# Optimization experiments

Measured on AMD Instinct MI355X. Metric: run time of the kernel, lower is better.

Reference implementation:

```python
import jax, jax.numpy as jnp
import numpy as np

N, K, R = 32768, 4096, 256

def setup_inputs() -> dict:
    key = jax.random.key(0)
    k1, k2, k3 = jax.random.split(key, 3)
    H = jax.random.normal(k1, (N, R), dtype=jnp.float32)
    L = jax.random.normal(k2, (K, R), dtype=jnp.float32)
    W_I = jax.random.normal(k3, (R, R), dtype=jnp.float32)
    return {"H": H, "L": L, "W_I": W_I}

def reference(H, L, W_I):
    # Q = W_I @ L^T : (r, k)
    Q = jnp.einsum('rs,ks->rk', W_I, L)
    # M_I = H @ Q : (n, k)
    M_I = jnp.einsum('nr,rk->nk', H, Q)
    A_I = jax.nn.softmax(M_I, axis=1)
    # C_I = A_I @ L : (n, r)
    C_I = jnp.einsum('nk,kr->nr', A_I, L)
    return (C_I, A_I)
```

## Files before the change

kernel.cpp:

```cpp
#include <hip/hip_runtime.h>
#include <hip/hip_bf16.h>
#include <math.h>
#include <stdint.h>

constexpr int N_ROWS = 32768;
constexpr int K_DIM  = 4096;
constexpr int R_DIM  = 256;
constexpr int KP     = 3 * R_DIM;
constexpr int KB     = K_DIM / 128;

typedef __bf16 bf16x8 __attribute__((ext_vector_type(8)));
typedef float  f32x4  __attribute__((ext_vector_type(4)));
typedef unsigned short u16x8 __attribute__((ext_vector_type(8)));
typedef unsigned short u16x4 __attribute__((ext_vector_type(4)));

__device__ __forceinline__ unsigned short f2bf(float x) {
    unsigned u = __float_as_uint(x);
    u += 0x7fffu + ((u >> 16) & 1u);
    return (unsigned short)(u >> 16);
}
__device__ __forceinline__ float bf2f(unsigned short h) {
    return __uint_as_float((unsigned)h << 16);
}

__device__ __forceinline__ void gl2lds16(const void* gptr, void* lptr) {
    __builtin_amdgcn_global_load_lds(
        (const __attribute__((address_space(1))) unsigned int*)gptr,
        (__attribute__((address_space(3))) unsigned int*)lptr,
        16, 0, 0);
}

__global__ __launch_bounds__(256)
void gemm_mfma_nt(const unsigned short* __restrict__ A,
                  const unsigned short* __restrict__ B,
                  float* __restrict__ C,
                  float* __restrict__ Pm, float* __restrict__ Ps,
                  int M, int N, int Kc)
{
    __shared__ __align__(16) unsigned short As[128 * 32];
    __shared__ __align__(16) unsigned short Bs[128 * 32];
    __shared__ float pm_s[128][2], ps_s[128][2];

    const int tid  = threadIdx.x;
    const int wave = tid >> 6, lane = tid & 63;
    const int wm = wave >> 1, wn = wave & 1;
    const long m0 = (long)blockIdx.x * 128;
    const long n0 = (long)blockIdx.y * 128;

    f32x4 acc[4][4] = {};

    const int srow  = lane >> 2;
    const int skoff = (lane & 3) * 8;
    const int c0 = wave, c1 = wave + 4;
    const int kq = (lane >> 4) * 8;
    const int mr = lane & 15;

    for (int k0 = 0; k0 < Kc; k0 += 32) {
        gl2lds16(A + (m0 + c0 * 16 + srow) * (long)Kc + k0 + skoff, &As[c0 * 512]);
        gl2lds16(A + (m0 + c1 * 16 + srow) * (long)Kc + k0 + skoff, &As[c1 * 512]);
        gl2lds16(B + (n0 + c0 * 16 + srow) * (long)Kc + k0 + skoff, &Bs[c0 * 512]);
        gl2lds16(B + (n0 + c1 * 16 + srow) * (long)Kc + k0 + skoff, &Bs[c1 * 512]);
        __syncthreads();

        bf16x8 af[4], bfr[4];
#pragma unroll
        for (int t = 0; t < 4; ++t) {
            af[t]  = *(const bf16x8*)&As[(wm * 64 + t * 16 + mr) * 32 + kq];
            bfr[t] = *(const bf16x8*)&Bs[(wn * 64 + t * 16 + mr) * 32 + kq];
        }
#pragma unroll
        for (int i = 0; i < 4; ++i)
#pragma unroll
            for (int j = 0; j < 4; ++j)
                acc[i][j] = __builtin_amdgcn_mfma_f32_16x16x32_bf16(
                    af[i], bfr[j], acc[i][j], 0, 0, 0);
        __syncthreads();
    }

    const int col = lane & 15, rquad = (lane >> 4) * 4;
#pragma unroll
    for (int i = 0; i < 4; ++i) {
        const long mrow = m0 + wm * 64 + i * 16 + rquad;
#pragma unroll
        for (int j = 0; j < 4; ++j) {
            float* p = C + mrow * (long)N + n0 + wn * 64 + j * 16 + col;
#pragma unroll
            for (int r = 0; r < 4; ++r) p[(long)r * N] = acc[i][j][r];
        }
    }

#pragma unroll
    for (int i = 0; i < 4; ++i) {
#pragma unroll
        for (int r = 0; r < 4; ++r) {
            float mx = fmaxf(fmaxf(acc[i][0][r], acc[i][1][r]),
                             fmaxf(acc[i][2][r], acc[i][3][r]));
#pragma unroll
            for (int off = 1; off < 16; off <<= 1)
                mx = fmaxf(mx, __shfl_xor(mx, off));
            float sm = 0.f;
#pragma unroll
            for (int j = 0; j < 4; ++j) sm += __expf(acc[i][j][r] - mx);
#pragma unroll
            for (int off = 1; off < 16; off <<= 1)
                sm += __shfl_xor(sm, off);
            if (mr == 0) {
                const int rw = wm * 64 + i * 16 + rquad + r;
                pm_s[rw][wn] = mx;
                ps_s[rw][wn] = sm;
            }
        }
    }
    __syncthreads();
    if (tid < 128) {
        const float ma = pm_s[tid][0], mb = pm_s[tid][1];
        const float mx = fmaxf(ma, mb);
        const float s  = ps_s[tid][0] * __expf(ma - mx) +
                         ps_s[tid][1] * __expf(mb - mx);
        Pm[(m0 + tid) * KB + blockIdx.y] = mx;
        Ps[(m0 + tid) * KB + blockIdx.y] = s;
    }
}

__global__ __launch_bounds__(256)
void finalize_ms(const float* __restrict__ Pm, const float* __restrict__ Ps,
                 float* __restrict__ SMm, float* __restrict__ SMi)
{
    const long row = (long)blockIdx.x * 256 + threadIdx.x;
    const float4* pm = (const float4*)(Pm + row * KB);
    const float4* ps = (const float4*)(Ps + row * KB);
    float4 v[8];
    float mx = -3.4e38f;
#pragma unroll
    for (int q = 0; q < 8; ++q) {
        v[q] = pm[q];
        mx = fmaxf(mx, fmaxf(fmaxf(v[q].x, v[q].y), fmaxf(v[q].z, v[q].w)));
    }
    float s = 0.f;
#pragma unroll
    for (int q = 0; q < 8; ++q) {
        float4 w = ps[q];
        s += w.x * __expf(v[q].x - mx) + w.y * __expf(v[q].y - mx) +
             w.z * __expf(v[q].z - mx) + w.w * __expf(v[q].w - mx);
    }
    SMm[row] = mx;
    SMi[row] = 1.f / s;
}

__global__ __launch_bounds__(256)
void softmax_av_sp(float* __restrict__ Mio,
                   const unsigned short* __restrict__ LT,
                   const float* __restrict__ SMm, const float* __restrict__ SMi,
                   float* __restrict__ C)
{
    __shared__ __align__(16) unsigned short Bs[2][R_DIM * 32];
    __shared__ __align__(16) unsigned short As[2][32 * 32];
    __shared__ float sm_m[32], sm_inv[32];

    const int tid  = threadIdx.x;
    const int wave = tid >> 6, lane = tid & 63;
    const long m0 = (long)blockIdx.x * 32;

    if (tid < 32) { sm_m[tid] = SMm[m0 + tid]; sm_inv[tid] = SMi[m0 + tid]; }
    __syncthreads();

    const int mr   = lane & 15;
    const int kq16 = (lane >> 4) * 16;
    const int arow = tid >> 3;
    const int acol = (tid & 7) * 4;
    const int abyte = (arow * 64 + (tid & 7) * 8) ^ ((arow & 3) << 4);
    const float myM = sm_m[arow], myI = sm_inv[arow];
    float* const arp = Mio + (m0 + arow) * (long)K_DIM + acol;

    f32x4 acc[2][4] = {};

    auto stage_B = [&](int buf, int kk0) {
#pragma unroll
        for (int w = 0; w < 4; ++w) {
            const int rloc = wave * 64 + w * 16 + (lane >> 2);
            const int sb   = ((lane & 3) * 16) ^ ((rloc & 3) << 4);
            gl2lds16((const char*)LT + (long)rloc * (K_DIM * 2) + (long)kk0 * 2 + sb,
                     &Bs[buf][(wave * 64 + w * 16) * 32]);
        }
    };
    auto emit_A = [&](int buf, int kk0, float4 v) {
        const float e0 = __expf(v.x - myM), e1 = __expf(v.y - myM);
        const float e2 = __expf(v.z - myM), e3 = __expf(v.w - myM);
        *(float4*)(arp + kk0) = make_float4(e0 * myI, e1 * myI, e2 * myI, e3 * myI);
        u16x4 u;
        u[0] = f2bf(e0); u[1] = f2bf(e1); u[2] = f2bf(e2); u[3] = f2bf(e3);
        *(u16x4*)((char*)As[buf] + abyte) = u;
    };

    stage_B(0, 0);
    emit_A(0, 0, *(const float4*)(arp + 0));
    __syncthreads();

    int cur = 0;
    for (int t = 0; t < K_DIM / 32; ++t) {
        const int nxt = cur ^ 1;
        float4 vn;
        const bool has_next = (t < K_DIM / 32 - 1);
        if (has_next) {
            stage_B(nxt, (t + 1) * 32);
            vn = *(const float4*)(arp + (t + 1) * 32);
        }

        bf16x8 af[2], bfr[4];
#pragma unroll
        for (int q = 0; q < 2; ++q) {
            const int ar = q * 16 + mr;
            af[q] = *(const bf16x8*)((const char*)As[cur] +
                    ((ar * 64 + kq16) ^ ((ar & 3) << 4)));
        }
#pragma unroll
        for (int q = 0; q < 4; ++q) {
            const int br = wave * 64 + q * 16 + mr;
            bfr[q] = *(const bf16x8*)((const char*)Bs[cur] +
                     ((br * 64 + kq16) ^ ((br & 3) << 4)));
        }
#pragma unroll
        for (int i = 0; i < 2; ++i)
#pragma unroll
            for (int j = 0; j < 4; ++j)
                acc[i][j] = __builtin_amdgcn_mfma_f32_16x16x32_bf16(
                    af[i], bfr[j], acc[i][j], 0, 0, 0);

        if (has_next) emit_A(nxt, (t + 1) * 32, vn);
        __syncthreads();
        cur = nxt;
    }

    const int col = lane & 15, rquad = (lane >> 4) * 4;
#pragma unroll
    for (int i = 0; i < 2; ++i) {
        const int lrow0 = i * 16 + rquad;
#pragma unroll
        for (int j = 0; j < 4; ++j) {
            float* p = C + (m0 + lrow0) * (long)R_DIM + wave * 64 + j * 16 + col;
#pragma unroll
            for (int r = 0; r < 4; ++r)
                p[(long)r * R_DIM] = acc[i][j][r] * sm_inv[lrow0 + r];
        }
    }
}

__global__ __launch_bounds__(256)
void prep_B(const float* __restrict__ L, unsigned short* __restrict__ Bp)
{
    const long i = (long)blockIdx.x * 256 + threadIdx.x;
    const long k = i >> 8; const int r = (int)(i & 255);
    const float x = L[i];
    const unsigned short hi = f2bf(x);
    const unsigned short lo = f2bf(x - bf2f(hi));
    unsigned short* row = Bp + k * KP;
    row[r] = hi; row[R_DIM + r] = lo; row[2 * R_DIM + r] = hi;
}

__global__ __launch_bounds__(256)
void prep_LT(const float* __restrict__ L, unsigned short* __restrict__ LT)
{
    const long i = (long)blockIdx.x * 256 + threadIdx.x;
    const long r = i >> 12; const long k = i & 4095;
    LT[r * K_DIM + k] = f2bf(L[k * R_DIM + r]);
}

template<bool BT>
__global__ __launch_bounds__(256)
void gemm128(const float* __restrict__ A, const float* __restrict__ B,
             float* __restrict__ C, int M, int N, int Kc)
{
    __shared__ __align__(16) float Asl[16][132];
    __shared__ __align__(16) float Bsl[16][132];

    const int tid = threadIdx.x;
    const int tx = tid & 15, ty = tid >> 4;
    const long m0 = (long)blockIdx.x * 128;
    const long n0 = (long)blockIdx.y * 128;

    float acc[8][8];
#pragma unroll
    for (int i = 0; i < 8; ++i)
#pragma unroll
        for (int j = 0; j < 8; ++j) acc[i][j] = 0.f;

    for (int k0 = 0; k0 < Kc; k0 += 16) {
#pragma unroll
        for (int q = 0; q < 2; ++q) {
            int fi = tid + 256 * q, row = fi >> 2, col = (fi & 3) * 4;
            float4 v = *(const float4*)(A + (m0 + row) * (long)Kc + k0 + col);
            Asl[col + 0][row] = v.x; Asl[col + 1][row] = v.y;
            Asl[col + 2][row] = v.z; Asl[col + 3][row] = v.w;
        }
        if (BT) {
#pragma unroll
            for (int q = 0; q < 2; ++q) {
                int fi = tid + 256 * q, row = fi >> 2, col = (fi & 3) * 4;
                float4 v = *(const float4*)(B + (n0 + row) * (long)Kc + k0 + col);
                Bsl[col + 0][row] = v.x; Bsl[col + 1][row] = v.y;
                Bsl[col + 2][row] = v.z; Bsl[col + 3][row] = v.w;
            }
        } else {
#pragma unroll
            for (int q = 0; q < 2; ++q) {
                int fi = tid + 256 * q, row = fi >> 5, col = (fi & 31) * 4;
                float4 v = *(const float4*)(B + (k0 + row) * (long)N + n0 + col);
                *(float4*)&Bsl[row][col] = v;
            }
        }
        __syncthreads();
#pragma unroll
        for (int kk = 0; kk < 16; ++kk) {
            float a[8], b[8];
            *(float4*)&a[0] = *(const float4*)&Asl[kk][ty * 8];
            *(float4*)&a[4] = *(const float4*)&Asl[kk][ty * 8 + 4];
            *(float4*)&b[0] = *(const float4*)&Bsl[kk][tx * 8];
            *(float4*)&b[4] = *(const float4*)&Bsl[kk][tx * 8 + 4];
#pragma unroll
            for (int i = 0; i < 8; ++i)
#pragma unroll
                for (int j = 0; j < 8; ++j)
                    acc[i][j] = fmaf(a[i], b[j], acc[i][j]);
        }
        __syncthreads();
    }
#pragma unroll
    for (int i = 0; i < 8; ++i) {
        float* p = C + (m0 + ty * 8 + i) * (long)N + n0 + tx * 8;
        *(float4*)p       = make_float4(acc[i][0], acc[i][1], acc[i][2], acc[i][3]);
        *(float4*)(p + 4) = make_float4(acc[i][4], acc[i][5], acc[i][6], acc[i][7]);
    }
}

__global__ __launch_bounds__(256)
void gemm128_hl(const float* __restrict__ A, const float* __restrict__ B,
                unsigned short* __restrict__ Ap, int M, int N, int Kc)
{
    __shared__ __align__(16) float Asl[16][132];
    __shared__ __align__(16) float Bsl[16][132];

    const int tid = threadIdx.x;
    const int tx = tid & 15, ty = tid >> 4;
    const long m0 = (long)blockIdx.x * 128;
    const long n0 = (long)blockIdx.y * 128;

    float acc[8][8];
#pragma unroll
    for (int i = 0; i < 8; ++i)
#pragma unroll
        for (int j = 0; j < 8; ++j) acc[i][j] = 0.f;

    for (int k0 = 0; k0 < Kc; k0 += 16) {
#pragma unroll
        for (int q = 0; q < 2; ++q) {
            int fi = tid + 256 * q, row = fi >> 2, col = (fi & 3) * 4;
            float4 v = *(const float4*)(A + (m0 + row) * (long)Kc + k0 + col);
            Asl[col + 0][row] = v.x; Asl[col + 1][row] = v.y;
            Asl[col + 2][row] = v.z; Asl[col + 3][row] = v.w;
        }
#pragma unroll
        for (int q = 0; q < 2; ++q) {
            int fi = tid + 256 * q, row = fi >> 5, col = (fi & 31) * 4;
            float4 v = *(const float4*)(B + (k0 + row) * (long)N + n0 + col);
            *(float4*)&Bsl[row][col] = v;
        }
        __syncthreads();
#pragma unroll
        for (int kk = 0; kk < 16; ++kk) {
            float a[8], b[8];
            *(float4*)&a[0] = *(const float4*)&Asl[kk][ty * 8];
            *(float4*)&a[4] = *(const float4*)&Asl[kk][ty * 8 + 4];
            *(float4*)&b[0] = *(const float4*)&Bsl[kk][tx * 8];
            *(float4*)&b[4] = *(const float4*)&Bsl[kk][tx * 8 + 4];
#pragma unroll
            for (int i = 0; i < 8; ++i)
#pragma unroll
                for (int j = 0; j < 8; ++j)
                    acc[i][j] = fmaf(a[i], b[j], acc[i][j]);
        }
        __syncthreads();
    }
#pragma unroll
    for (int i = 0; i < 8; ++i) {
        const long row = m0 + ty * 8 + i;
        const int  cb  = (int)n0 + tx * 8;
        u16x8 vh, vl;
#pragma unroll
        for (int j = 0; j < 8; ++j) {
            const float x = acc[i][j];
            const unsigned short hi = f2bf(x);
            vh[j] = hi;
            vl[j] = f2bf(x - bf2f(hi));
        }
        unsigned short* rp = Ap + row * KP;
        *(u16x8*)(rp + cb)             = vh;
        *(u16x8*)(rp + R_DIM + cb)     = vh;
        *(u16x8*)(rp + 2 * R_DIM + cb) = vl;
    }
}

__global__ __launch_bounds__(256)
void softmax_rows(float* __restrict__ Mio)
{
    const long n  = blockIdx.x;
    float* row    = Mio + n * (long)K_DIM;
    const int tid = threadIdx.x;

    float4 v[4];
    float lmax = -3.4e38f;
#pragma unroll
    for (int q = 0; q < 4; ++q) {
        v[q] = ((const float4*)row)[tid + 256 * q];
        lmax = fmaxf(lmax, fmaxf(fmaxf(v[q].x, v[q].y), fmaxf(v[q].z, v[q].w)));
    }
    __shared__ float redmax[4], redsum[4];
#pragma unroll
    for (int off = 32; off > 0; off >>= 1)
        lmax = fmaxf(lmax, __shfl_xor(lmax, off));
    if ((tid & 63) == 0) redmax[tid >> 6] = lmax;
    __syncthreads();
    const float gmax = fmaxf(fmaxf(redmax[0], redmax[1]), fmaxf(redmax[2], redmax[3]));

    float lsum = 0.f;
#pragma unroll
    for (int q = 0; q < 4; ++q) {
        v[q].x = __expf(v[q].x - gmax); v[q].y = __expf(v[q].y - gmax);
        v[q].z = __expf(v[q].z - gmax); v[q].w = __expf(v[q].w - gmax);
        lsum += v[q].x + v[q].y + v[q].z + v[q].w;
    }
#pragma unroll
    for (int off = 32; off > 0; off >>= 1)
        lsum += __shfl_xor(lsum, off);
    if ((tid & 63) == 0) redsum[tid >> 6] = lsum;
    __syncthreads();
    const float inv = 1.f / (redsum[0] + redsum[1] + redsum[2] + redsum[3]);
#pragma unroll
    for (int q = 0; q < 4; ++q) {
        v[q].x *= inv; v[q].y *= inv; v[q].z *= inv; v[q].w *= inv;
        ((float4*)row)[tid + 256 * q] = v[q];
    }
}

extern "C" void kernel_launch(void* const* d_in, const int* in_sizes, int n_in,
                              void* d_out, int out_size, void* d_ws, size_t ws_size,
                              hipStream_t stream)
{
    const float* H  = (const float*)d_in[0];
    const float* L  = (const float*)d_in[1];
    const float* Wi = (const float*)d_in[2];

    float* Cout = (float*)d_out;
    float* Aout = (float*)d_out + (size_t)N_ROWS * R_DIM;

    const size_t szAp = (size_t)N_ROWS * KP * 2;
    const size_t szBp = (size_t)K_DIM * KP * 2;
    const size_t szLT = (size_t)R_DIM * K_DIM * 2;
    const size_t szPm = (size_t)N_ROWS * KB * 4;
    const size_t szPs = (size_t)N_ROWS * KB * 4;
    const size_t szSM = (size_t)N_ROWS * 4;

    if (ws_size >= szAp + szBp + szLT + szPm + szPs + 2 * szSM) {
        char* w = (char*)d_ws;
        unsigned short* Ap = (unsigned short*)w;                 w += szAp;
        unsigned short* Bp = (unsigned short*)w;                 w += szBp;
        unsigned short* LT = (unsigned short*)w;                 w += szLT;
        float* Pm  = (float*)w;                                  w += szPm;
        float* Ps  = (float*)w;                                  w += szPs;
        float* SMm = (float*)w;                                  w += szSM;
        float* SMi = (float*)w;

        gemm128_hl<<<dim3(N_ROWS / 128, R_DIM / 128), 256, 0, stream>>>(
            H, Wi, Ap, N_ROWS, R_DIM, R_DIM);
        prep_B<<<dim3((K_DIM * R_DIM) / 256), 256, 0, stream>>>(L, Bp);
        prep_LT<<<dim3((R_DIM * K_DIM) / 256), 256, 0, stream>>>(L, LT);
        gemm_mfma_nt<<<dim3(N_ROWS / 128, K_DIM / 128), 256, 0, stream>>>(
            Ap, Bp, Aout, Pm, Ps, N_ROWS, K_DIM, KP);
        finalize_ms<<<dim3(N_ROWS / 256), 256, 0, stream>>>(Pm, Ps, SMm, SMi);
        softmax_av_sp<<<dim3(N_ROWS / 32), 256, 0, stream>>>(
            Aout, LT, SMm, SMi, Cout);
    } else {
        gemm128<false><<<dim3(N_ROWS / 128, R_DIM / 128), 256, 0, stream>>>(
            H, Wi, Cout, N_ROWS, R_DIM, R_DIM);
        gemm128<true><<<dim3(N_ROWS / 128, K_DIM / 128), 256, 0, stream>>>(
            Cout, L, Aout, N_ROWS, K_DIM, R_DIM);
        softmax_rows<<<dim3(N_ROWS), 256, 0, stream>>>(Aout);
        gemm128<false><<<dim3(N_ROWS / 128, R_DIM / 128), 256, 0, stream>>>(
            Aout, L, Cout, N_ROWS, R_DIM, K_DIM);
    }
}
```

Measured before the change: 1.359 ms.

## Load B operands directly from global memory and widen softmax-AV tiles

The first GEMM no longer stages the small B matrix in LDS. Each wave loads its B fragments straight from global memory, which relies on L2 reuse, and the grid is swapped so blocks sharing an A row-tile run together. The softmax-AV kernel moves to 512 threads covering 64 rows and 64-wide K steps. It also drops the LDS staging of L^T in favour of direct global loads, cutting LDS traffic and barriers per step. The risk is uncoalesced, latency-exposed global loads for B in place of the shared-memory reuse.

```diff
diff --git a/kernel.cpp b/kernel.cpp
--- a/kernel.cpp
+++ b/kernel.cpp
@@ -38,14 +38,13 @@
                   int M, int N, int Kc)
 {
     __shared__ __align__(16) unsigned short As[128 * 32];
-    __shared__ __align__(16) unsigned short Bs[128 * 32];
     __shared__ float pm_s[128][2], ps_s[128][2];
 
     const int tid  = threadIdx.x;
     const int wave = tid >> 6, lane = tid & 63;
     const int wm = wave >> 1, wn = wave & 1;
-    const long m0 = (long)blockIdx.x * 128;
-    const long n0 = (long)blockIdx.y * 128;
+    const long m0 = (long)blockIdx.y * 128;
+    const long n0 = (long)blockIdx.x * 128;
 
     f32x4 acc[4][4] = {};
 
@@ -55,19 +54,23 @@
     const int kq = (lane >> 4) * 8;
     const int mr = lane & 15;
 
+    const unsigned short* const Bbase = B + n0 * (long)Kc + kq;
+
     for (int k0 = 0; k0 < Kc; k0 += 32) {
         gl2lds16(A + (m0 + c0 * 16 + srow) * (long)Kc + k0 + skoff, &As[c0 * 512]);
         gl2lds16(A + (m0 + c1 * 16 + srow) * (long)Kc + k0 + skoff, &As[c1 * 512]);
-        gl2lds16(B + (n0 + c0 * 16 + srow) * (long)Kc + k0 + skoff, &Bs[c0 * 512]);
-        gl2lds16(B + (n0 + c1 * 16 + srow) * (long)Kc + k0 + skoff, &Bs[c1 * 512]);
-        __syncthreads();
-
-        bf16x8 af[4], bfr[4];
-#pragma unroll
-        for (int t = 0; t < 4; ++t) {
-            af[t]  = *(const bf16x8*)&As[(wm * 64 + t * 16 + mr) * 32 + kq];
-            bfr[t] = *(const bf16x8*)&Bs[(wn * 64 + t * 16 + mr) * 32 + kq];
-        }
+
+        bf16x8 bfr[4];
+#pragma unroll
+        for (int t = 0; t < 4; ++t)
+            bfr[t] = *(const bf16x8*)(Bbase + (wn * 64 + t * 16 + mr) * (long)Kc + k0);
+
+        __syncthreads();
+
+        bf16x8 af[4];
+#pragma unroll
+        for (int t = 0; t < 4; ++t)
+            af[t] = *(const bf16x8*)&As[(wm * 64 + t * 16 + mr) * 32 + kq];
 #pragma unroll
         for (int i = 0; i < 4; ++i)
 #pragma unroll
@@ -117,8 +120,8 @@
         const float mx = fmaxf(ma, mb);
         const float s  = ps_s[tid][0] * __expf(ma - mx) +
                          ps_s[tid][1] * __expf(mb - mx);
-        Pm[(m0 + tid) * KB + blockIdx.y] = mx;
-        Ps[(m0 + tid) * KB + blockIdx.y] = s;
+        Pm[(m0 + tid) * KB + blockIdx.x] = mx;
+        Ps[(m0 + tid) * KB + blockIdx.x] = s;
     }
 }
 
@@ -147,86 +150,88 @@
     SMi[row] = 1.f / s;
 }
 
-__global__ __launch_bounds__(256)
-void softmax_av_sp(float* __restrict__ Mio,
-                   const unsigned short* __restrict__ LT,
-                   const float* __restrict__ SMm, const float* __restrict__ SMi,
-                   float* __restrict__ C)
-{
-    __shared__ __align__(16) unsigned short Bs[2][R_DIM * 32];
-    __shared__ __align__(16) unsigned short As[2][32 * 32];
-    __shared__ float sm_m[32], sm_inv[32];
+__global__ __launch_bounds__(512)
+void softmax_av2(float* __restrict__ Mio,
+                 const unsigned short* __restrict__ LT,
+                 const float* __restrict__ SMm, const float* __restrict__ SMi,
+                 float* __restrict__ C)
+{
+    __shared__ __align__(16) unsigned short As[2][64 * 64];
+    __shared__ float sm_m[64], sm_inv[64];
 
     const int tid  = threadIdx.x;
     const int wave = tid >> 6, lane = tid & 63;
-    const long m0 = (long)blockIdx.x * 32;
-
-    if (tid < 32) { sm_m[tid] = SMm[m0 + tid]; sm_inv[tid] = SMi[m0 + tid]; }
+    const long m0 = (long)blockIdx.x * 64;
+
+    if (tid < 64) { sm_m[tid] = SMm[m0 + tid]; sm_inv[tid] = SMi[m0 + tid]; }
     __syncthreads();
 
-    const int mr   = lane & 15;
+    const int wm = wave >> 2, wn = wave & 3;
+    const int mr = lane & 15;
+    const int kq   = (lane >> 4) * 8;
     const int kq16 = (lane >> 4) * 16;
-    const int arow = tid >> 3;
-    const int acol = (tid & 7) * 4;
-    const int abyte = (arow * 64 + (tid & 7) * 8) ^ ((arow & 3) << 4);
+
+    const int arow  = tid >> 3;
+    const int abyte = (arow * 128 + (tid & 7) * 16) ^ ((arow & 7) << 4);
     const float myM = sm_m[arow], myI = sm_inv[arow];
-    float* const arp = Mio + (m0 + arow) * (long)K_DIM + acol;
+    float* const arp = Mio + (m0 + arow) * (long)K_DIM + (tid & 7) * 8;
+
+    const unsigned short* const Lbase = LT + (wn * 64) * (long)K_DIM + kq;
 
     f32x4 acc[2][4] = {};
 
-    auto stage_B = [&](int buf, int kk0) {
-#pragma unroll
-        for (int w = 0; w < 4; ++w) {
-            const int rloc = wave * 64 + w * 16 + (lane >> 2);
-            const int sb   = ((lane & 3) * 16) ^ ((rloc & 3) << 4);
-            gl2lds16((const char*)LT + (long)rloc * (K_DIM * 2) + (long)kk0 * 2 + sb,
-                     &Bs[buf][(wave * 64 + w * 16) * 32]);
-        }
+    auto emit_A = [&](int buf, int kk0, float4 v0, float4 v1) {
+        float e0 = __expf(v0.x - myM), e1 = __expf(v0.y - myM);
+        float e2 = __expf(v0.z - myM), e3 = __expf(v0.w - myM);
+        float e4 = __expf(v1.x - myM), e5 = __expf(v1.y - myM);
+        float e6 = __expf(v1.z - myM), e7 = __expf(v1.w - myM);
+        *(float4*)(arp + kk0)     = make_float4(e0*myI, e1*myI, e2*myI, e3*myI);
+        *(float4*)(arp + kk0 + 4) = make_float4(e4*myI, e5*myI, e6*myI, e7*myI);
+        u16x8 u;
+        u[0]=f2bf(e0); u[1]=f2bf(e1); u[2]=f2bf(e2); u[3]=f2bf(e3);
+        u[4]=f2bf(e4); u[5]=f2bf(e5); u[6]=f2bf(e6); u[7]=f2bf(e7);
+        *(u16x8*)((char*)As[buf] + abyte) = u;
     };
-    auto emit_A = [&](int buf, int kk0, float4 v) {
-        const float e0 = __expf(v.x - myM), e1 = __expf(v.y - myM);
-        const float e2 = __expf(v.z - myM), e3 = __expf(v.w - myM);
-        *(float4*)(arp + kk0) = make_float4(e0 * myI, e1 * myI, e2 * myI, e3 * myI);
-        u16x4 u;
-        u[0] = f2bf(e0); u[1] = f2bf(e1); u[2] = f2bf(e2); u[3] = f2bf(e3);
-        *(u16x4*)((char*)As[buf] + abyte) = u;
-    };
-
-    stage_B(0, 0);
-    emit_A(0, 0, *(const float4*)(arp + 0));
+
+    emit_A(0, 0, *(const float4*)arp, *(const float4*)(arp + 4));
     __syncthreads();
 
     int cur = 0;
-    for (int t = 0; t < K_DIM / 32; ++t) {
+    for (int t = 0; t < K_DIM / 64; ++t) {
         const int nxt = cur ^ 1;
-        float4 vn;
-        const bool has_next = (t < K_DIM / 32 - 1);
+        const bool has_next = (t + 1 < K_DIM / 64);
+        float4 v0, v1;
         if (has_next) {
-            stage_B(nxt, (t + 1) * 32);
-            vn = *(const float4*)(arp + (t + 1) * 32);
-        }
-
-        bf16x8 af[2], bfr[4];
-#pragma unroll
-        for (int q = 0; q < 2; ++q) {
-            const int ar = q * 16 + mr;
-            af[q] = *(const bf16x8*)((const char*)As[cur] +
-                    ((ar * 64 + kq16) ^ ((ar & 3) << 4)));
-        }
-#pragma unroll
-        for (int q = 0; q < 4; ++q) {
-            const int br = wave * 64 + q * 16 + mr;
-            bfr[q] = *(const bf16x8*)((const char*)Bs[cur] +
-                     ((br * 64 + kq16) ^ ((br & 3) << 4)));
-        }
-#pragma unroll
-        for (int i = 0; i < 2; ++i)
-#pragma unroll
-            for (int j = 0; j < 4; ++j)
-                acc[i][j] = __builtin_amdgcn_mfma_f32_16x16x32_bf16(
-                    af[i], bfr[j], acc[i][j], 0, 0, 0);
-
-        if (has_next) emit_A(nxt, (t + 1) * 32, vn);
+            v0 = *(const float4*)(arp + (t + 1) * 64);
+            v1 = *(const float4*)(arp + (t + 1) * 64 + 4);
+        }
+
+        bf16x8 bfr[2][4];
+#pragma unroll
+        for (int ks = 0; ks < 2; ++ks)
+#pragma unroll
+            for (int q = 0; q < 4; ++q)
+                bfr[ks][q] = *(const bf16x8*)(Lbase + (q * 16 + mr) * (long)K_DIM
+                                              + t * 64 + ks * 32);
+        bf16x8 af[2][2];
+#pragma unroll
+        for (int ks = 0; ks < 2; ++ks)
+#pragma unroll
+            for (int q = 0; q < 2; ++q) {
+                const int ar = wm * 32 + q * 16 + mr;
+                af[ks][q] = *(const bf16x8*)((const char*)As[cur] +
+                            ((ar * 128 + ks * 64 + kq16) ^ ((ar & 7) << 4)));
+            }
+#pragma unroll
+        for (int ks = 0; ks < 2; ++ks)
+#pragma unroll
+            for (int i = 0; i < 2; ++i)
+#pragma unroll
+                for (int j = 0; j < 4; ++j)
+                    acc[i][j] = __builtin_amdgcn_mfma_f32_16x16x32_bf16(
+                        af[ks][i], bfr[ks][j], acc[i][j], 0, 0, 0);
+
+        if (has_next) emit_A(nxt, (t + 1) * 64, v0, v1);
         __syncthreads();
         cur = nxt;
     }
@@ -234,10 +239,10 @@
     const int col = lane & 15, rquad = (lane >> 4) * 4;
 #pragma unroll
     for (int i = 0; i < 2; ++i) {
-        const int lrow0 = i * 16 + rquad;
+        const int lrow0 = wm * 32 + i * 16 + rquad;
 #pragma unroll
         for (int j = 0; j < 4; ++j) {
-            float* p = C + (m0 + lrow0) * (long)R_DIM + wave * 64 + j * 16 + col;
+            float* p = C + (m0 + lrow0) * (long)R_DIM + wn * 64 + j * 16 + col;
 #pragma unroll
             for (int r = 0; r < 4; ++r)
                 p[(long)r * R_DIM] = acc[i][j][r] * sm_inv[lrow0 + r];
@@ -473,10 +478,10 @@
             H, Wi, Ap, N_ROWS, R_DIM, R_DIM);
         prep_B<<<dim3((K_DIM * R_DIM) / 256), 256, 0, stream>>>(L, Bp);
         prep_LT<<<dim3((R_DIM * K_DIM) / 256), 256, 0, stream>>>(L, LT);
-        gemm_mfma_nt<<<dim3(N_ROWS / 128, K_DIM / 128), 256, 0, stream>>>(
+        gemm_mfma_nt<<<dim3(K_DIM / 128, N_ROWS / 128), 256, 0, stream>>>(
             Ap, Bp, Aout, Pm, Ps, N_ROWS, K_DIM, KP);
         finalize_ms<<<dim3(N_ROWS / 256), 256, 0, stream>>>(Pm, Ps, SMm, SMi);
-        softmax_av_sp<<<dim3(N_ROWS / 32), 256, 0, stream>>>(
+        softmax_av2<<<dim3(N_ROWS / 64), 512, 0, stream>>>(
             Aout, LT, SMm, SMi, Cout);
     } else {
         gemm128<false><<<dim3(N_ROWS / 128, R_DIM / 128), 256, 0, stream>>>(
```

Result: slower. 1.449 ms (+6.6%).

## Split fused softmax-AV into exp pass plus wide GEMM, widen logit GEMM K-tile

Applied to the files above, without the earlier changes.

The logit GEMM now stages 64-wide K tiles with an XOR-swizzled LDS layout, which halves the barrier count and avoids bank conflicts. The fused softmax+A·L kernel is replaced by two kernels. A standalone exp_apply pass normalizes the attention matrix in place. A 512-thread GEMM then reads the normalized fp32 probabilities, converts them to bf16 on the fly, and multiplies by L^T using 128-row tiles that span all 256 output columns. This trades an extra full read/write pass over the 512MB attention matrix for better MFMA tiling and occupancy in the second GEMM, and it loses the double buffering the old kernel had.

```diff
diff --git a/kernel.cpp b/kernel.cpp
--- a/kernel.cpp
+++ b/kernel.cpp
@@ -12,7 +12,6 @@
 typedef __bf16 bf16x8 __attribute__((ext_vector_type(8)));
 typedef float  f32x4  __attribute__((ext_vector_type(4)));
 typedef unsigned short u16x8 __attribute__((ext_vector_type(8)));
-typedef unsigned short u16x4 __attribute__((ext_vector_type(4)));
 
 __device__ __forceinline__ unsigned short f2bf(float x) {
     unsigned u = __float_as_uint(x);
@@ -31,14 +30,14 @@
 }
 
 __global__ __launch_bounds__(256)
-void gemm_mfma_nt(const unsigned short* __restrict__ A,
-                  const unsigned short* __restrict__ B,
-                  float* __restrict__ C,
-                  float* __restrict__ Pm, float* __restrict__ Ps,
-                  int M, int N, int Kc)
-{
-    __shared__ __align__(16) unsigned short As[128 * 32];
-    __shared__ __align__(16) unsigned short Bs[128 * 32];
+void gemm_mfma_nt2(const unsigned short* __restrict__ A,
+                   const unsigned short* __restrict__ B,
+                   float* __restrict__ C,
+                   float* __restrict__ Pm, float* __restrict__ Ps,
+                   int M, int N, int Kc)
+{
+    __shared__ __align__(16) unsigned short As[128 * 64];
+    __shared__ __align__(16) unsigned short Bs[128 * 64];
     __shared__ float pm_s[128][2], ps_s[128][2];
 
     const int tid  = threadIdx.x;
@@ -49,31 +48,40 @@
 
     f32x4 acc[4][4] = {};
 
-    const int srow  = lane >> 2;
-    const int skoff = (lane & 3) * 8;
-    const int c0 = wave, c1 = wave + 4;
-    const int kq = (lane >> 4) * 8;
+    const int lrow  = lane >> 3;
+    const int loffE = ((((lane & 7) * 16) ^ (lrow << 4)) >> 1);
+    const int kq16 = (lane >> 4) * 16;
     const int mr = lane & 15;
 
-    for (int k0 = 0; k0 < Kc; k0 += 32) {
-        gl2lds16(A + (m0 + c0 * 16 + srow) * (long)Kc + k0 + skoff, &As[c0 * 512]);
-        gl2lds16(A + (m0 + c1 * 16 + srow) * (long)Kc + k0 + skoff, &As[c1 * 512]);
-        gl2lds16(B + (n0 + c0 * 16 + srow) * (long)Kc + k0 + skoff, &Bs[c0 * 512]);
-        gl2lds16(B + (n0 + c1 * 16 + srow) * (long)Kc + k0 + skoff, &Bs[c1 * 512]);
-        __syncthreads();
-
-        bf16x8 af[4], bfr[4];
-#pragma unroll
-        for (int t = 0; t < 4; ++t) {
-            af[t]  = *(const bf16x8*)&As[(wm * 64 + t * 16 + mr) * 32 + kq];
-            bfr[t] = *(const bf16x8*)&Bs[(wn * 64 + t * 16 + mr) * 32 + kq];
-        }
-#pragma unroll
-        for (int i = 0; i < 4; ++i)
-#pragma unroll
-            for (int j = 0; j < 4; ++j)
-                acc[i][j] = __builtin_amdgcn_mfma_f32_16x16x32_bf16(
-                    af[i], bfr[j], acc[i][j], 0, 0, 0);
+    for (int k0 = 0; k0 < Kc; k0 += 64) {
+#pragma unroll
+        for (int c = 0; c < 4; ++c) {
+            const int ch = wave * 4 + c;
+            gl2lds16(A + (m0 + ch * 8 + lrow) * (long)Kc + k0 + loffE, &As[ch * 512]);
+            gl2lds16(B + (n0 + ch * 8 + lrow) * (long)Kc + k0 + loffE, &Bs[ch * 512]);
+        }
+        __syncthreads();
+
+        bf16x8 af[2][4], bfr[2][4];
+#pragma unroll
+        for (int ks = 0; ks < 2; ++ks)
+#pragma unroll
+            for (int t = 0; t < 4; ++t) {
+                const int ar = wm * 64 + t * 16 + mr;
+                const int br = wn * 64 + t * 16 + mr;
+                af[ks][t]  = *(const bf16x8*)((const char*)As +
+                             (ar * 128 + ((ks * 64 + kq16) ^ ((ar & 7) << 4))));
+                bfr[ks][t] = *(const bf16x8*)((const char*)Bs +
+                             (br * 128 + ((ks * 64 + kq16) ^ ((br & 7) << 4))));
+            }
+#pragma unroll
+        for (int ks = 0; ks < 2; ++ks)
+#pragma unroll
+            for (int i = 0; i < 4; ++i)
+#pragma unroll
+                for (int j = 0; j < 4; ++j)
+                    acc[i][j] = __builtin_amdgcn_mfma_f32_16x16x32_bf16(
+                        af[ks][i], bfr[ks][j], acc[i][j], 0, 0, 0);
         __syncthreads();
     }
 
@@ -148,99 +156,89 @@
 }
 
 __global__ __launch_bounds__(256)
-void softmax_av_sp(float* __restrict__ Mio,
-                   const unsigned short* __restrict__ LT,
-                   const float* __restrict__ SMm, const float* __restrict__ SMi,
-                   float* __restrict__ C)
-{
-    __shared__ __align__(16) unsigned short Bs[2][R_DIM * 32];
-    __shared__ __align__(16) unsigned short As[2][32 * 32];
-    __shared__ float sm_m[32], sm_inv[32];
+void exp_apply(float* __restrict__ Mio,
+               const float* __restrict__ SMm, const float* __restrict__ SMi)
+{
+    const int tid = threadIdx.x;
+    const long r0 = (long)blockIdx.x * 8;
+#pragma unroll
+    for (int r = 0; r < 8; ++r) {
+        const long row = r0 + r;
+        const float m = SMm[row], inv = SMi[row];
+        float4* p = (float4*)(Mio + row * (long)K_DIM);
+#pragma unroll
+        for (int it = 0; it < 4; ++it) {
+            float4 v = p[it * 256 + tid];
+            v.x = __expf(v.x - m) * inv;
+            v.y = __expf(v.y - m) * inv;
+            v.z = __expf(v.z - m) * inv;
+            v.w = __expf(v.w - m) * inv;
+            p[it * 256 + tid] = v;
+        }
+    }
+}
+
+__global__ __launch_bounds__(512)
+void gemm_a32_w(const float* __restrict__ A,
+                const unsigned short* __restrict__ LT,
+                float* __restrict__ C)
+{
+    __shared__ __align__(16) unsigned short As[128 * 32];
+    __shared__ __align__(16) unsigned short Bs[256 * 32];
 
     const int tid  = threadIdx.x;
     const int wave = tid >> 6, lane = tid & 63;
-    const long m0 = (long)blockIdx.x * 32;
-
-    if (tid < 32) { sm_m[tid] = SMm[m0 + tid]; sm_inv[tid] = SMi[m0 + tid]; }
-    __syncthreads();
-
-    const int mr   = lane & 15;
-    const int kq16 = (lane >> 4) * 16;
-    const int arow = tid >> 3;
-    const int acol = (tid & 7) * 4;
-    const int abyte = (arow * 64 + (tid & 7) * 8) ^ ((arow & 3) << 4);
-    const float myM = sm_m[arow], myI = sm_inv[arow];
-    float* const arp = Mio + (m0 + arow) * (long)K_DIM + acol;
-
-    f32x4 acc[2][4] = {};
-
-    auto stage_B = [&](int buf, int kk0) {
-#pragma unroll
-        for (int w = 0; w < 4; ++w) {
-            const int rloc = wave * 64 + w * 16 + (lane >> 2);
-            const int sb   = ((lane & 3) * 16) ^ ((rloc & 3) << 4);
-            gl2lds16((const char*)LT + (long)rloc * (K_DIM * 2) + (long)kk0 * 2 + sb,
-                     &Bs[buf][(wave * 64 + w * 16) * 32]);
-        }
-    };
-    auto emit_A = [&](int buf, int kk0, float4 v) {
-        const float e0 = __expf(v.x - myM), e1 = __expf(v.y - myM);
-        const float e2 = __expf(v.z - myM), e3 = __expf(v.w - myM);
-        *(float4*)(arp + kk0) = make_float4(e0 * myI, e1 * myI, e2 * myI, e3 * myI);
-        u16x4 u;
-        u[0] = f2bf(e0); u[1] = f2bf(e1); u[2] = f2bf(e2); u[3] = f2bf(e3);
-        *(u16x4*)((char*)As[buf] + abyte) = u;
-    };
-
-    stage_B(0, 0);
-    emit_A(0, 0, *(const float4*)(arp + 0));
-    __syncthreads();
-
-    int cur = 0;
-    for (int t = 0; t < K_DIM / 32; ++t) {
-        const int nxt = cur ^ 1;
-        float4 vn;
-        const bool has_next = (t < K_DIM / 32 - 1);
-        if (has_next) {
-            stage_B(nxt, (t + 1) * 32);
-            vn = *(const float4*)(arp + (t + 1) * 32);
-        }
-
-        bf16x8 af[2], bfr[4];
-#pragma unroll
-        for (int q = 0; q < 2; ++q) {
-            const int ar = q * 16 + mr;
-            af[q] = *(const bf16x8*)((const char*)As[cur] +
-                    ((ar * 64 + kq16) ^ ((ar & 3) << 4)));
-        }
-#pragma unroll
-        for (int q = 0; q < 4; ++q) {
-            const int br = wave * 64 + q * 16 + mr;
-            bfr[q] = *(const bf16x8*)((const char*)Bs[cur] +
-                     ((br * 64 + kq16) ^ ((br & 3) << 4)));
-        }
-#pragma unroll
-        for (int i = 0; i < 2; ++i)
+    const int wm = wave >> 2, wn = wave & 3;
+    const long m0 = (long)blockIdx.x * 128;
+
+    f32x4 acc[4][4] = {};
+
+    const int kq = (lane >> 4) * 8;
+    const int mr = lane & 15;
+    const int arow = tid >> 2, acol = (tid & 3) * 8;
+    const int srow = lane >> 2, skoff = (lane & 3) * 8;
+
+    for (int k0 = 0; k0 < K_DIM; k0 += 32) {
+#pragma unroll
+        for (int c = 0; c < 2; ++c) {
+            const int ch = wave * 2 + c;
+            gl2lds16(LT + (ch * 16 + srow) * (long)K_DIM + k0 + skoff, &Bs[ch * 512]);
+        }
+        {
+            const float* g = A + (m0 + arow) * (long)K_DIM + k0 + acol;
+            float4 v0 = *(const float4*)(g + 0);
+            float4 v1 = *(const float4*)(g + 4);
+            u16x8 u;
+            u[0] = f2bf(v0.x); u[1] = f2bf(v0.y); u[2] = f2bf(v0.z); u[3] = f2bf(v0.w);
+            u[4] = f2bf(v1.x); u[5] = f2bf(v1.y); u[6] = f2bf(v1.z); u[7] = f2bf(v1.w);
+            *(u16x8*)&As[arow * 32 + acol] = u;
+        }
+        __syncthreads();
+
+        bf16x8 af[4], bfr[4];
+#pragma unroll
+        for (int t = 0; t < 4; ++t) {
+            af[t]  = *(const bf16x8*)&As[(wm * 64 + t * 16 + mr) * 32 + kq];
+            bfr[t] = *(const bf16x8*)&Bs[(wn * 64 + t * 16 + mr) * 32 + kq];
+        }
+#pragma unroll
+        for (int i = 0; i < 4; ++i)
 #pragma unroll
             for (int j = 0; j < 4; ++j)
                 acc[i][j] = __builtin_amdgcn_mfma_f32_16x16x32_bf16(
                     af[i], bfr[j], acc[i][j], 0, 0, 0);
-
-        if (has_next) emit_A(nxt, (t + 1) * 32, vn);
-        __syncthreads();
-        cur = nxt;
+        __syncthreads();
     }
 
     const int col = lane & 15, rquad = (lane >> 4) * 4;
 #pragma unroll
-    for (int i = 0; i < 2; ++i) {
-        const int lrow0 = i * 16 + rquad;
+    for (int i = 0; i < 4; ++i) {
+        const long mrow = m0 + wm * 64 + i * 16 + rquad;
 #pragma unroll
         for (int j = 0; j < 4; ++j) {
-            float* p = C + (m0 + lrow0) * (long)R_DIM + wave * 64 + j * 16 + col;
-#pragma unroll
-            for (int r = 0; r < 4; ++r)
-                p[(long)r * R_DIM] = acc[i][j][r] * sm_inv[lrow0 + r];
+            float* p = C + mrow * (long)R_DIM + wn * 64 + j * 16 + col;
+#pragma unroll
+            for (int r = 0; r < 4; ++r) p[(long)r * R_DIM] = acc[i][j][r];
         }
     }
 }
@@ -473,11 +471,11 @@
             H, Wi, Ap, N_ROWS, R_DIM, R_DIM);
         prep_B<<<dim3((K_DIM * R_DIM) / 256), 256, 0, stream>>>(L, Bp);
         prep_LT<<<dim3((R_DIM * K_DIM) / 256), 256, 0, stream>>>(L, LT);
-        gemm_mfma_nt<<<dim3(N_ROWS / 128, K_DIM / 128), 256, 0, stream>>>(
+        gemm_mfma_nt2<<<dim3(N_ROWS / 128, K_DIM / 128), 256, 0, stream>>>(
             Ap, Bp, Aout, Pm, Ps, N_ROWS, K_DIM, KP);
         finalize_ms<<<dim3(N_ROWS / 256), 256, 0, stream>>>(Pm, Ps, SMm, SMi);
-        softmax_av_sp<<<dim3(N_ROWS / 32), 256, 0, stream>>>(
-            Aout, LT, SMm, SMi, Cout);
+        exp_apply<<<dim3(N_ROWS / 8), 256, 0, stream>>>(Aout, SMm, SMi);
+        gemm_a32_w<<<dim3(N_ROWS / 128), 512, 0, stream>>>(Aout, LT, Cout);
     } else {
         gemm128<false><<<dim3(N_ROWS / 128, R_DIM / 128), 256, 0, stream>>>(
             H, Wi, Cout, N_ROWS, R_DIM, R_DIM);
```

New measurement: 1.414 ms. +4.0%, slower.

## Enlarge softmax-AV tile to 64 rows with 8 waves, single-buffered K=64 steps

Applied to the files above, without the earlier changes.

Restructures the softmax-normalize plus A·L kernel to process 64 rows per block with 512 threads arranged as a 2x4 wave grid, and to step through K in chunks of 64 instead of 32. Each staged L^T tile is now reused across twice as many rows, which halves the global/L2 traffic for B per output row and halves the number of K iterations and barriers. In exchange, the double-buffered software pipeline is dropped: loads and exp work are followed by a sync before compute, so memory latency is less hidden, and the larger block may lower occupancy.

```diff
diff --git a/kernel.cpp b/kernel.cpp
--- a/kernel.cpp
+++ b/kernel.cpp
@@ -147,97 +147,87 @@
     SMi[row] = 1.f / s;
 }
 
-__global__ __launch_bounds__(256)
-void softmax_av_sp(float* __restrict__ Mio,
+__global__ __launch_bounds__(512)
+void softmax_av_pv(float* __restrict__ Mio,
                    const unsigned short* __restrict__ LT,
                    const float* __restrict__ SMm, const float* __restrict__ SMi,
                    float* __restrict__ C)
 {
-    __shared__ __align__(16) unsigned short Bs[2][R_DIM * 32];
-    __shared__ __align__(16) unsigned short As[2][32 * 32];
-    __shared__ float sm_m[32], sm_inv[32];
+    __shared__ __align__(16) unsigned short Bs[R_DIM * 64];
+    __shared__ __align__(16) unsigned short As[64 * 64];
+    __shared__ float sm_m[64], sm_inv[64];
 
     const int tid  = threadIdx.x;
     const int wave = tid >> 6, lane = tid & 63;
-    const long m0 = (long)blockIdx.x * 32;
-
-    if (tid < 32) { sm_m[tid] = SMm[m0 + tid]; sm_inv[tid] = SMi[m0 + tid]; }
+    const long m0 = (long)blockIdx.x * 64;
+
+    if (tid < 64) { sm_m[tid] = SMm[m0 + tid]; sm_inv[tid] = SMi[m0 + tid]; }
     __syncthreads();
 
-    const int mr   = lane & 15;
+    f32x4 acc[2][4] = {};
+    const int wm = wave >> 2, wn = wave & 3;
+    const int mr = lane & 15;
     const int kq16 = (lane >> 4) * 16;
-    const int arow = tid >> 3;
-    const int acol = (tid & 7) * 4;
-    const int abyte = (arow * 64 + (tid & 7) * 8) ^ ((arow & 3) << 4);
-    const float myM = sm_m[arow], myI = sm_inv[arow];
-    float* const arp = Mio + (m0 + arow) * (long)K_DIM + acol;
-
-    f32x4 acc[2][4] = {};
-
-    auto stage_B = [&](int buf, int kk0) {
-#pragma unroll
-        for (int w = 0; w < 4; ++w) {
-            const int rloc = wave * 64 + w * 16 + (lane >> 2);
-            const int sb   = ((lane & 3) * 16) ^ ((rloc & 3) << 4);
-            gl2lds16((const char*)LT + (long)rloc * (K_DIM * 2) + (long)kk0 * 2 + sb,
-                     &Bs[buf][(wave * 64 + w * 16) * 32]);
-        }
-    };
-    auto emit_A = [&](int buf, int kk0, float4 v) {
-        const float e0 = __expf(v.x - myM), e1 = __expf(v.y - myM);
-        const float e2 = __expf(v.z - myM), e3 = __expf(v.w - myM);
-        *(float4*)(arp + kk0) = make_float4(e0 * myI, e1 * myI, e2 * myI, e3 * myI);
-        u16x4 u;
-        u[0] = f2bf(e0); u[1] = f2bf(e1); u[2] = f2bf(e2); u[3] = f2bf(e3);
-        *(u16x4*)((char*)As[buf] + abyte) = u;
-    };
-
-    stage_B(0, 0);
-    emit_A(0, 0, *(const float4*)(arp + 0));
-    __syncthreads();
-
-    int cur = 0;
-    for (int t = 0; t < K_DIM / 32; ++t) {
-        const int nxt = cur ^ 1;
-        float4 vn;
-        const bool has_next = (t < K_DIM / 32 - 1);
-        if (has_next) {
-            stage_B(nxt, (t + 1) * 32);
-            vn = *(const float4*)(arp + (t + 1) * 32);
-        }
-
-        bf16x8 af[2], bfr[4];
-#pragma unroll
-        for (int q = 0; q < 2; ++q) {
-            const int ar = q * 16 + mr;
-            af[q] = *(const bf16x8*)((const char*)As[cur] +
-                    ((ar * 64 + kq16) ^ ((ar & 3) << 4)));
-        }
+
+    for (int k0 = 0; k0 < K_DIM; k0 += 64) {
 #pragma unroll
         for (int q = 0; q < 4; ++q) {
-            const int br = wave * 64 + q * 16 + mr;
-            bfr[q] = *(const bf16x8*)((const char*)Bs[cur] +
-                     ((br * 64 + kq16) ^ ((br & 3) << 4)));
-        }
-#pragma unroll
-        for (int i = 0; i < 2; ++i)
-#pragma unroll
-            for (int j = 0; j < 4; ++j)
-                acc[i][j] = __builtin_amdgcn_mfma_f32_16x16x32_bf16(
-                    af[i], bfr[j], acc[i][j], 0, 0, 0);
-
-        if (has_next) emit_A(nxt, (t + 1) * 32, vn);
-        __syncthreads();
-        cur = nxt;
+            const int rbase = q * 64 + wave * 8;
+            const int rloc  = rbase + (lane >> 3);
+            const int phys  = (lane & 7) * 16;
+            const int kbyte = phys ^ ((rloc & 7) << 4);
+            gl2lds16((const char*)LT + (long)rloc * (K_DIM * 2) + (long)k0 * 2 + kbyte,
+                     &Bs[rbase * 64]);
+        }
+#pragma unroll
+        for (int p = 0; p < 2; ++p) {
+            const int row = p * 32 + wave * 4 + (lane >> 4);
+            const int col = (lane & 15) * 4;
+            float* gp = Mio + (m0 + row) * (long)K_DIM + k0 + col;
+            float4 v = *(const float4*)gp;
+            const float mrow = sm_m[row], inv = sm_inv[row];
+            float e0 = __expf(v.x - mrow), e1 = __expf(v.y - mrow);
+            float e2 = __expf(v.z - mrow), e3 = __expf(v.w - mrow);
+            *(float4*)gp = make_float4(e0 * inv, e1 * inv, e2 * inv, e3 * inv);
+            u16x4 u;
+            u[0] = f2bf(e0); u[1] = f2bf(e1); u[2] = f2bf(e2); u[3] = f2bf(e3);
+            const int byte = (row * 128 + col * 2) ^ ((row & 7) << 4);
+            *(u16x4*)((char*)As + byte) = u;
+        }
+        __syncthreads();
+
+#pragma unroll
+        for (int ks = 0; ks < 2; ++ks) {
+            bf16x8 af[2], bfr[4];
+#pragma unroll
+            for (int t = 0; t < 2; ++t) {
+                const int arow = wm * 32 + t * 16 + mr;
+                const int ab = (arow * 128 + ks * 64 + kq16) ^ ((arow & 7) << 4);
+                af[t] = *(const bf16x8*)((const char*)As + ab);
+            }
+#pragma unroll
+            for (int t = 0; t < 4; ++t) {
+                const int brow = wn * 64 + t * 16 + mr;
+                const int bb = (brow * 128 + ks * 64 + kq16) ^ ((brow & 7) << 4);
+                bfr[t] = *(const bf16x8*)((const char*)Bs + bb);
+            }
+#pragma unroll
+            for (int i = 0; i < 2; ++i)
+#pragma unroll
+                for (int j = 0; j < 4; ++j)
+                    acc[i][j] = __builtin_amdgcn_mfma_f32_16x16x32_bf16(
+                        af[i], bfr[j], acc[i][j], 0, 0, 0);
+        }
+        __syncthreads();
     }
 
     const int col = lane & 15, rquad = (lane >> 4) * 4;
 #pragma unroll
     for (int i = 0; i < 2; ++i) {
-        const int lrow0 = i * 16 + rquad;
+        const int lrow0 = wm * 32 + i * 16 + rquad;
 #pragma unroll
         for (int j = 0; j < 4; ++j) {
-            float* p = C + (m0 + lrow0) * (long)R_DIM + wave * 64 + j * 16 + col;
+            float* p = C + (m0 + lrow0) * (long)R_DIM + wn * 64 + j * 16 + col;
 #pragma unroll
             for (int r = 0; r < 4; ++r)
                 p[(long)r * R_DIM] = acc[i][j][r] * sm_inv[lrow0 + r];
@@ -476,7 +466,7 @@
         gemm_mfma_nt<<<dim3(N_ROWS / 128, K_DIM / 128), 256, 0, stream>>>(
             Ap, Bp, Aout, Pm, Ps, N_ROWS, K_DIM, KP);
         finalize_ms<<<dim3(N_ROWS / 256), 256, 0, stream>>>(Pm, Ps, SMm, SMi);
-        softmax_av_sp<<<dim3(N_ROWS / 32), 256, 0, stream>>>(
+        softmax_av_pv<<<dim3(N_ROWS / 64), 512, 0, stream>>>(
             Aout, LT, SMm, SMi, Cout);
     } else {
         gemm128<false><<<dim3(N_ROWS / 128, R_DIM / 128), 256, 0, stream>>>(
```

New measurement: 1.256 ms. 1.08x faster.
